# Performance work log

Measured on AMD Instinct MI355X. Metric: run time of the kernel, lower is better.

The kernel has to match this reference:

```python
import jax, jax.numpy as jnp
import numpy as np

D_MODEL = 1024
NUM_HEADS = 16
HEAD_DIM = D_MODEL // NUM_HEADS
WINDOW = 256
NEG = -1000000000.0


def setup_inputs() -> dict:
    key = jax.random.key(0)
    ks = jax.random.split(key, 9)
    B, N, D = 2, 2048, D_MODEL
    s = 1.0 / np.sqrt(D)
    inp = {
        "x": jax.random.normal(ks[0], (B, N, D), dtype=jnp.float32),
        "Wq": jax.random.normal(ks[1], (D, D), dtype=jnp.float32) * s,
        "bq": jnp.zeros((D,), dtype=jnp.float32),
        "Wk": jax.random.normal(ks[2], (D, D), dtype=jnp.float32) * s,
        "bk": jnp.zeros((D,), dtype=jnp.float32),
        "Wv": jax.random.normal(ks[3], (D, D), dtype=jnp.float32) * s,
        "bv": jnp.zeros((D,), dtype=jnp.float32),
        "Wo": jax.random.normal(ks[4], (D, D), dtype=jnp.float32) * s,
        "bo": jnp.zeros((D,), dtype=jnp.float32),
    }
    return inp


def reference(x, Wq, bq, Wk, bk, Wv, bv, Wo, bo):
    B, N, D = x.shape
    H, hd = NUM_HEADS, HEAD_DIM
    q = (x @ Wq + bq).reshape(B, N, H, hd).transpose(0, 2, 1, 3)  # [B,H,N,hd]
    k = (x @ Wk + bk).reshape(B, N, H, hd).transpose(0, 2, 1, 3)
    v = (x @ Wv + bv).reshape(B, N, H, hd).transpose(0, 2, 1, 3)

    i = jnp.arange(N)[:, None]
    j = jnp.arange(N)[None, :]
    blocked = (j > i) | (j < i - WINDOW)  # causal + local window
    mask = jnp.where(blocked, jnp.float32(NEG), jnp.float32(0.0))  # [N,N]

    logits = jnp.einsum("bhid,bhjd->bhij", q, k) / jnp.sqrt(jnp.float32(hd))
    logits = logits + mask[None, None, :, :]
    attn = jax.nn.softmax(logits, axis=-1)
    out = jnp.einsum("bhij,bhjd->bhid", attn, v)  # [B,H,N,hd]
    out = out.transpose(0, 2, 1, 3).reshape(B, N, D)
    return out @ Wo + bo
```

## Files before the change

kernel.cpp:

```cpp
#include <hip/hip_runtime.h>


typedef unsigned short ushort_t;
typedef __bf16 bf16x8 __attribute__((ext_vector_type(8)));
typedef float f32x4 __attribute__((ext_vector_type(4)));
typedef unsigned short ushort8 __attribute__((ext_vector_type(8)));

#define LOG2E 1.4426950408889634f

static __device__ __forceinline__ ushort_t f2b(float f) {
    union { float f; unsigned int u; } x;
    x.f = f;
    unsigned int u = x.u;
    unsigned int r = (u + 0x7FFFu + ((u >> 16) & 1u)) >> 16;
    return (ushort_t)r;
}

static __device__ __forceinline__ void store_out(float* p, float v) { *p = v; }
static __device__ __forceinline__ void store_out(ushort_t* p, float v) { *p = f2b(v); }

static __device__ __forceinline__ void gload_lds16(const ushort_t* g, ushort_t* l) {
    __builtin_amdgcn_global_load_lds(
        (const __attribute__((address_space(1))) void*)g,
        (__attribute__((address_space(3))) void*)l, 16, 0, 0);
}

__global__ __launch_bounds__(256) void cast_f32_bf16_kernel(
    const float* __restrict__ in, ushort_t* __restrict__ out) {
    int i = (blockIdx.x * 256 + threadIdx.x) * 8;
    f32x4 a = *(const f32x4*)&in[i];
    f32x4 b = *(const f32x4*)&in[i + 4];
    ushort8 o;
#pragma unroll
    for (int e = 0; e < 4; e++) o[e] = f2b(a[e]);
#pragma unroll
    for (int e = 0; e < 4; e++) o[4 + e] = f2b(b[e]);
    *(ushort8*)&out[i] = o;
}

__global__ __launch_bounds__(256) void transpose_cast_kernel(
    const float* __restrict__ W0, const float* __restrict__ W1,
    const float* __restrict__ W2, const float* __restrict__ W3,
    ushort_t* __restrict__ T0, ushort_t* __restrict__ T1,
    ushort_t* __restrict__ T2, ushort_t* __restrict__ T3) {
    __shared__ ushort_t tile[32][33];
    const float* W;
    ushort_t* T;
    switch (blockIdx.z) {
        case 0: W = W0; T = T0; break;
        case 1: W = W1; T = T1; break;
        case 2: W = W2; T = T2; break;
        default: W = W3; T = T3; break;
    }
    int tx = threadIdx.x, ty = threadIdx.y;
    int x = blockIdx.x * 32 + tx;
    int ybase = blockIdx.y * 32 + ty;
#pragma unroll
    for (int r = 0; r < 4; r++) tile[ty + r * 8][tx] = f2b(W[(ybase + r * 8) * 1024 + x]);
    __syncthreads();
    int xo = blockIdx.y * 32 + tx;
    int yobase = blockIdx.x * 32 + ty;
#pragma unroll
    for (int r = 0; r < 4; r++) T[(yobase + r * 8) * 1024 + xo] = tile[tx][ty + r * 8];
}

template <typename OutT, int MF, int NF>
__global__ __launch_bounds__(256) void gemm_bt_kernel(
    const ushort_t* __restrict__ A,
    const ushort_t* __restrict__ Bt0, const ushort_t* __restrict__ Bt1,
    const ushort_t* __restrict__ Bt2,
    const float* __restrict__ bias0, const float* __restrict__ bias1,
    const float* __restrict__ bias2,
    OutT* __restrict__ C0, OutT* __restrict__ C1, OutT* __restrict__ C2,
    float os0, float os1, float os2) {
    __shared__ ushort_t Al[MF * 32 * 64];
    __shared__ ushort_t Bl[NF * 32 * 64];

    const ushort_t* Bt;
    const float* bias;
    OutT* C;
    float oscale;
    if (blockIdx.z == 0) { Bt = Bt0; bias = bias0; C = C0; oscale = os0; }
    else if (blockIdx.z == 1) { Bt = Bt1; bias = bias1; C = C1; oscale = os1; }
    else { Bt = Bt2; bias = bias2; C = C2; oscale = os2; }

    const int m0 = blockIdx.y * (MF * 32);
    const int n0 = blockIdx.x * (NF * 32);
    const int tid = threadIdx.x;
    const int w = tid >> 6;
    const int l = tid & 63;
    const int wm = (w >> 1) * (MF * 16);
    const int wn = (w & 1) * (NF * 16);
    const int lrow = l & 15;
    const int lq = l >> 4;

    f32x4 acc[MF][NF];
#pragma unroll
    for (int mi = 0; mi < MF; mi++)
#pragma unroll
        for (int ni = 0; ni < NF; ni++) acc[mi][ni] = 0.0f;

    for (int kt = 0; kt < 1024; kt += 64) {
#pragma unroll
        for (int t = 0; t < MF; t++) {
            int idx = t * 256 + tid;
            gload_lds16(&A[(long)(m0 + (idx >> 3)) * 1024 + kt + (idx & 7) * 8], &Al[idx * 8]);
        }
#pragma unroll
        for (int t = 0; t < NF; t++) {
            int idx = t * 256 + tid;
            gload_lds16(&Bt[(long)(n0 + (idx >> 3)) * 1024 + kt + (idx & 7) * 8], &Bl[idx * 8]);
        }
        __syncthreads();
#pragma unroll
        for (int ks = 0; ks < 64; ks += 32) {
            bf16x8 af[MF], bfr[NF];
#pragma unroll
            for (int mi = 0; mi < MF; mi++)
                af[mi] = *(const bf16x8*)&Al[(wm + mi * 16 + lrow) * 64 + ks + lq * 8];
#pragma unroll
            for (int ni = 0; ni < NF; ni++)
                bfr[ni] = *(const bf16x8*)&Bl[(wn + ni * 16 + lrow) * 64 + ks + lq * 8];
#pragma unroll
            for (int mi = 0; mi < MF; mi++)
#pragma unroll
                for (int ni = 0; ni < NF; ni++)
                    acc[mi][ni] = __builtin_amdgcn_mfma_f32_16x16x32_bf16(
                        af[mi], bfr[ni], acc[mi][ni], 0, 0, 0);
        }
        __syncthreads();
    }

#pragma unroll
    for (int ni = 0; ni < NF; ni++) {
        int n = n0 + wn + ni * 16 + lrow;
        float bv = bias[n];
#pragma unroll
        for (int mi = 0; mi < MF; mi++) {
#pragma unroll
            for (int r = 0; r < 4; r++) {
                int m = m0 + wm + mi * 16 + lq * 4 + r;
                store_out(&C[(long)m * 1024 + n], (acc[mi][ni][r] + bv) * oscale);
            }
        }
    }
}

__global__ __launch_bounds__(256) void attn_kernel(
    const ushort_t* __restrict__ Q, const ushort_t* __restrict__ K,
    const ushort_t* __restrict__ V, ushort_t* __restrict__ O) {
    __shared__ ushort_t Kl[128 * 64];
    __shared__ ushort_t Vt[64 * 136];
    __shared__ ushort_t Pb[4 * 16 * 40];

    const int b = blockIdx.z;
    const int h = blockIdx.y;
    const int i0 = blockIdx.x * 64;
    const int tid = threadIdx.x;
    const int w = tid >> 6;
    const int l = tid & 63;
    const int lrow = l & 15;
    const int lq = l >> 4;
    const int q0 = i0 + w * 16;

    const long baseBH = ((long)b * 2048) * 1024 + (long)h * 64;

    const ushort_t* qrow = Q + baseBH + (long)(q0 + lrow) * 1024;
    bf16x8 aq0 = *(const bf16x8*)&qrow[lq * 8];
    bf16x8 aq1 = *(const bf16x8*)&qrow[32 + lq * 8];

    float lpart[4];
    f32x4 oacc[4];
#pragma unroll
    for (int r = 0; r < 4; r++) lpart[r] = 0.0f;
#pragma unroll
    for (int ni = 0; ni < 4; ni++) oacc[ni] = 0.0f;

    const int kstart = (i0 - 256) > 0 ? (i0 - 256) : 0;
    const int kend = i0 + 64;
    ushort_t* Pw = &Pb[w * 16 * 40];

    for (int cs = kstart; cs < kend; cs += 128) {
        const int ce = (cs + 128 < kend) ? cs + 128 : kend;
        const int rows = ce - cs;
#pragma unroll
        for (int t = 0; t < 4; t++) {
            int idx = t * 256 + tid;
            int rr = idx >> 3;
            int cc = (idx & 7) * 8;
            if (rr < rows)
                *(ushort8*)&Kl[idx * 8] = *(const ushort8*)&K[baseBH + (long)(cs + rr) * 1024 + cc];
        }
        {
            int rr = tid >> 1;
            int ch = (tid & 1) * 32;
            if (rr < rows) {
                const ushort_t* vrow = V + baseBH + (long)(cs + rr) * 1024 + ch;
#pragma unroll
                for (int g = 0; g < 4; g++) {
                    ushort8 vv = *(const ushort8*)&vrow[g * 8];
#pragma unroll
                    for (int e = 0; e < 8; e++) Vt[(ch + g * 8 + e) * 136 + rr] = vv[e];
                }
            }
        }
        __syncthreads();

        for (int kb = cs; kb < ce; kb += 32) {
            if (kb > q0 + 15 || kb + 31 < q0 - 256) continue;
            const int rb = kb - cs;
            f32x4 S0 = 0.0f, S1 = 0.0f;
            {
                bf16x8 bk;
                bk = *(const bf16x8*)&Kl[(rb + lrow) * 64 + lq * 8];
                S0 = __builtin_amdgcn_mfma_f32_16x16x32_bf16(aq0, bk, S0, 0, 0, 0);
                bk = *(const bf16x8*)&Kl[(rb + lrow) * 64 + 32 + lq * 8];
                S0 = __builtin_amdgcn_mfma_f32_16x16x32_bf16(aq1, bk, S0, 0, 0, 0);
                bk = *(const bf16x8*)&Kl[(rb + 16 + lrow) * 64 + lq * 8];
                S1 = __builtin_amdgcn_mfma_f32_16x16x32_bf16(aq0, bk, S1, 0, 0, 0);
                bk = *(const bf16x8*)&Kl[(rb + 16 + lrow) * 64 + 32 + lq * 8];
                S1 = __builtin_amdgcn_mfma_f32_16x16x32_bf16(aq1, bk, S1, 0, 0, 0);
            }
            const int col0 = kb + lrow;
            const int col1 = kb + 16 + lrow;
#pragma unroll
            for (int r = 0; r < 4; r++) {
                const int i = q0 + lq * 4 + r;
                float p0 = (col0 > i || col0 < i - 256) ? 0.0f : exp2f(S0[r] * LOG2E);
                float p1 = (col1 > i || col1 < i - 256) ? 0.0f : exp2f(S1[r] * LOG2E);
                lpart[r] += p0 + p1;
                const int prow = lq * 4 + r;
                Pw[prow * 40 + lrow] = f2b(p0);
                Pw[prow * 40 + 16 + lrow] = f2b(p1);
            }
            bf16x8 pf = *(const bf16x8*)&Pw[lrow * 40 + lq * 8];
#pragma unroll
            for (int ni = 0; ni < 4; ni++) {
                bf16x8 vf = *(const bf16x8*)&Vt[(ni * 16 + lrow) * 136 + rb + lq * 8];
                oacc[ni] = __builtin_amdgcn_mfma_f32_16x16x32_bf16(pf, vf, oacc[ni], 0, 0, 0);
            }
        }
        __syncthreads();
    }

    float lS[4];
#pragma unroll
    for (int r = 0; r < 4; r++) {
        float rs = lpart[r];
#pragma unroll
        for (int off = 8; off; off >>= 1) rs += __shfl_xor(rs, off, 64);
        lS[r] = rs;
    }

#pragma unroll
    for (int ni = 0; ni < 4; ni++) {
#pragma unroll
        for (int r = 0; r < 4; r++) {
            const int i = q0 + lq * 4 + r;
            const int d = ni * 16 + lrow;
            O[baseBH + (long)i * 1024 + d] = f2b(oacc[ni][r] / lS[r]);
        }
    }
}

extern "C" void kernel_launch(void* const* d_in, const int* in_sizes, int n_in,
                              void* d_out, int out_size, void* d_ws, size_t ws_size,
                              hipStream_t stream) {
    const float* x  = (const float*)d_in[0];
    const float* Wq = (const float*)d_in[1];
    const float* bq = (const float*)d_in[2];
    const float* Wk = (const float*)d_in[3];
    const float* bk = (const float*)d_in[4];
    const float* Wv = (const float*)d_in[5];
    const float* bv = (const float*)d_in[6];
    const float* Wo = (const float*)d_in[7];
    const float* bo = (const float*)d_in[8];
    float* out = (float*)d_out;

    ushort_t* ws = (ushort_t*)d_ws;
    const size_t WMAT = (size_t)1024 * 1024;
    const size_t ACT = (size_t)2 * 2048 * 1024;
    ushort_t* xbf = ws;
    ushort_t* Wqt = xbf + ACT;
    ushort_t* Wkt = Wqt + WMAT;
    ushort_t* Wvt = Wkt + WMAT;
    ushort_t* Wot = Wvt + WMAT;
    ushort_t* qws = Wot + WMAT;
    ushort_t* kws = qws + ACT;
    ushort_t* vws = kws + ACT;
    ushort_t* aws = xbf;

    cast_f32_bf16_kernel<<<dim3((unsigned)(ACT / 2048)), 256, 0, stream>>>(x, xbf);

    transpose_cast_kernel<<<dim3(32, 32, 4), dim3(32, 8), 0, stream>>>(
        Wq, Wk, Wv, Wo, Wqt, Wkt, Wvt, Wot);

    gemm_bt_kernel<ushort_t, 2, 4><<<dim3(8, 64, 3), 256, 0, stream>>>(
        xbf, Wqt, Wkt, Wvt, bq, bk, bv, qws, kws, vws, 0.125f, 1.0f, 1.0f);

    attn_kernel<<<dim3(32, 16, 2), 256, 0, stream>>>(qws, kws, vws, aws);

    gemm_bt_kernel<float, 2, 2><<<dim3(16, 64, 1), 256, 0, stream>>>(
        aws, Wot, Wot, Wot, bo, bo, bo, out, out, out, 1.0f, 1.0f, 1.0f);
}
```

Before: 185.9 us.

## Remap GEMM and attention blocks per XCD, widen output-projection tiles

The GEMM and attention grids become 1D launches whose block IDs are decoded so that consecutive blocks on the same XCD (id & 7) share row or head ranges. The goal is more L2 reuse of A tiles, weight tiles and K/V within each XCD's private cache. The output-projection GEMM also moves from 64x64 tiles to the same 64x128 tile as the QKV GEMM, which halves its block count and raises per-block reuse. In exchange, the mapping relies on blocks being dispatched round-robin across XCDs, and the output GEMM has fewer blocks to fill the GPU.

```diff
diff --git a/kernel.cpp b/kernel.cpp
--- a/kernel.cpp
+++ b/kernel.cpp
@@ -64,7 +64,7 @@
     for (int r = 0; r < 4; r++) T[(yobase + r * 8) * 1024 + xo] = tile[tx][ty + r * 8];
 }
 
-template <typename OutT, int MF, int NF>
+template <typename OutT, int MODE>
 __global__ __launch_bounds__(256) void gemm_bt_kernel(
     const ushort_t* __restrict__ A,
     const ushort_t* __restrict__ Bt0, const ushort_t* __restrict__ Bt1,
@@ -73,58 +73,73 @@
     const float* __restrict__ bias2,
     OutT* __restrict__ C0, OutT* __restrict__ C1, OutT* __restrict__ C2,
     float os0, float os1, float os2) {
-    __shared__ ushort_t Al[MF * 32 * 64];
-    __shared__ ushort_t Bl[NF * 32 * 64];
+    __shared__ ushort_t Al[64 * 64];
+    __shared__ ushort_t Bl[128 * 64];
+
+    const int id = blockIdx.x;
+    const int xcd = id & 7;
+    const int s = id >> 3;
+    int m_blk, ncol, zsel;
+    if (MODE == 0) {
+        m_blk = (xcd >> 1) * 16 + (s & 15);
+        ncol = (xcd & 1) * 12 + (s >> 4);
+        zsel = ncol >> 3;
+        ncol &= 7;
+    } else {
+        m_blk = xcd * 8 + (s & 7);
+        ncol = s >> 3;
+        zsel = 0;
+    }
+    const int m0 = m_blk * 64;
+    const int n0 = ncol * 128;
 
     const ushort_t* Bt;
     const float* bias;
     OutT* C;
     float oscale;
-    if (blockIdx.z == 0) { Bt = Bt0; bias = bias0; C = C0; oscale = os0; }
-    else if (blockIdx.z == 1) { Bt = Bt1; bias = bias1; C = C1; oscale = os1; }
+    if (zsel == 0) { Bt = Bt0; bias = bias0; C = C0; oscale = os0; }
+    else if (zsel == 1) { Bt = Bt1; bias = bias1; C = C1; oscale = os1; }
     else { Bt = Bt2; bias = bias2; C = C2; oscale = os2; }
 
-    const int m0 = blockIdx.y * (MF * 32);
-    const int n0 = blockIdx.x * (NF * 32);
     const int tid = threadIdx.x;
     const int w = tid >> 6;
     const int l = tid & 63;
-    const int wm = (w >> 1) * (MF * 16);
-    const int wn = (w & 1) * (NF * 16);
+    const int wm = (w >> 1) * 32;
+    const int wn = (w & 1) * 64;
     const int lrow = l & 15;
     const int lq = l >> 4;
 
-    f32x4 acc[MF][NF];
-#pragma unroll
-    for (int mi = 0; mi < MF; mi++)
-#pragma unroll
-        for (int ni = 0; ni < NF; ni++) acc[mi][ni] = 0.0f;
+    f32x4 acc[2][4];
+#pragma unroll
+    for (int mi = 0; mi < 2; mi++)
+#pragma unroll
+        for (int ni = 0; ni < 4; ni++) acc[mi][ni] = 0.0f;
 
     for (int kt = 0; kt < 1024; kt += 64) {
 #pragma unroll
-        for (int t = 0; t < MF; t++) {
+        for (int t = 0; t < 2; t++) {
             int idx = t * 256 + tid;
             gload_lds16(&A[(long)(m0 + (idx >> 3)) * 1024 + kt + (idx & 7) * 8], &Al[idx * 8]);
         }
 #pragma unroll
-        for (int t = 0; t < NF; t++) {
+        for (int t = 0; t < 4; t++) {
             int idx = t * 256 + tid;
             gload_lds16(&Bt[(long)(n0 + (idx >> 3)) * 1024 + kt + (idx & 7) * 8], &Bl[idx * 8]);
         }
         __syncthreads();
 #pragma unroll
         for (int ks = 0; ks < 64; ks += 32) {
-            bf16x8 af[MF], bfr[NF];
-#pragma unroll
-            for (int mi = 0; mi < MF; mi++)
+            bf16x8 af[2], bfr[4];
+#pragma unroll
+            for (int mi = 0; mi < 2; mi++)
                 af[mi] = *(const bf16x8*)&Al[(wm + mi * 16 + lrow) * 64 + ks + lq * 8];
 #pragma unroll
-            for (int ni = 0; ni < NF; ni++)
+            for (int ni = 0; ni < 4; ni++)
                 bfr[ni] = *(const bf16x8*)&Bl[(wn + ni * 16 + lrow) * 64 + ks + lq * 8];
 #pragma unroll
-            for (int mi = 0; mi < MF; mi++)
-#pragma unroll
-                for (int ni = 0; ni < NF; ni++)
+            for (int mi = 0; mi < 2; mi++)
+#pragma unroll
+                for (int ni = 0; ni < 4; ni++)
                     acc[mi][ni] = __builtin_amdgcn_mfma_f32_16x16x32_bf16(
                         af[mi], bfr[ni], acc[mi][ni], 0, 0, 0);
         }
@@ -132,11 +147,11 @@
     }
 
 #pragma unroll
-    for (int ni = 0; ni < NF; ni++) {
+    for (int ni = 0; ni < 4; ni++) {
         int n = n0 + wn + ni * 16 + lrow;
         float bv = bias[n];
 #pragma unroll
-        for (int mi = 0; mi < MF; mi++) {
+        for (int mi = 0; mi < 2; mi++) {
 #pragma unroll
             for (int r = 0; r < 4; r++) {
                 int m = m0 + wm + mi * 16 + lq * 4 + r;
@@ -153,9 +168,14 @@
     __shared__ ushort_t Vt[64 * 136];
     __shared__ ushort_t Pb[4 * 16 * 40];
 
-    const int b = blockIdx.z;
-    const int h = blockIdx.y;
-    const int i0 = blockIdx.x * 64;
+    const int id = blockIdx.x;
+    const int xcd = id & 7;
+    const int s = id >> 3;
+    const int bh = xcd * 4 + (s >> 5);
+    const int b = bh >> 4;
+    const int h = bh & 15;
+    const int i0 = (s & 31) * 64;
+
     const int tid = threadIdx.x;
     const int w = tid >> 6;
     const int l = tid & 63;
@@ -295,11 +315,11 @@
     transpose_cast_kernel<<<dim3(32, 32, 4), dim3(32, 8), 0, stream>>>(
         Wq, Wk, Wv, Wo, Wqt, Wkt, Wvt, Wot);
 
-    gemm_bt_kernel<ushort_t, 2, 4><<<dim3(8, 64, 3), 256, 0, stream>>>(
+    gemm_bt_kernel<ushort_t, 0><<<1536, 256, 0, stream>>>(
         xbf, Wqt, Wkt, Wvt, bq, bk, bv, qws, kws, vws, 0.125f, 1.0f, 1.0f);
 
-    attn_kernel<<<dim3(32, 16, 2), 256, 0, stream>>>(qws, kws, vws, aws);
-
-    gemm_bt_kernel<float, 2, 2><<<dim3(16, 64, 1), 256, 0, stream>>>(
+    attn_kernel<<<1024, 256, 0, stream>>>(qws, kws, vws, aws);
+
+    gemm_bt_kernel<float, 1><<<512, 256, 0, stream>>>(
         aws, Wot, Wot, Wot, bo, bo, bo, out, out, out, 1.0f, 1.0f, 1.0f);
 }
```

Result: faster. 178.9 us (-3.8%).
